# Kernel tuning notes

Measured on AMD Instinct MI355X. Metric: run time of the kernel, lower is better.

## Reference

```python
import jax, jax.numpy as jnp
import numpy as np

DIM = 1024
HEADS = 16
HEAD_DIM = DIM // HEADS
B, S = 4, 2048


def setup_inputs() -> dict:
    key = jax.random.key(0)
    ks = jax.random.split(key, 10)
    std = 1.0 / np.sqrt(DIM)
    def lin(k):
        kw, kb = jax.random.split(k)
        W = jax.random.uniform(kw, (DIM, DIM), jnp.float32, -std, std)
        b = jax.random.uniform(kb, (DIM,), jnp.float32, -std, std)
        return W, b
    Wq, bq = lin(ks[0])
    Wk, bk = lin(ks[1])
    Wv, bv = lin(ks[2])
    Wo, bo = lin(ks[3])
    q = jax.random.normal(ks[4], (B, S, DIM), jnp.float32)
    mask = jnp.ones((B, S), dtype=bool)
    return {"q": q, "mask": mask, "Wq": Wq, "bq": bq, "Wk": Wk, "bk": bk,
            "Wv": Wv, "bv": bv, "Wo": Wo, "bo": bo}


def reference(q, mask, Wq, bq, Wk, bk, Wv, bv, Wo, bo):
    # self-attention: k = v = q
    Bsz, Sq, D = q.shape
    scale = HEAD_DIM ** -0.5
    qh = (q @ Wq.T + bq).reshape(Bsz, Sq, HEADS, HEAD_DIM)
    kh = (q @ Wk.T + bk).reshape(Bsz, Sq, HEADS, HEAD_DIM)
    vh = (q @ Wv.T + bv).reshape(Bsz, Sq, HEADS, HEAD_DIM)
    # scores: [B, H, Sq, Sk]
    scores = jnp.einsum('bqhd,bkhd->bhqk', qh, kh) * scale
    neg_inf = jnp.finfo(scores.dtype).min
    # padding mask (batch, seq) -> broadcast over heads and query dim
    scores = jnp.where(mask[:, None, None, :], scores, neg_inf)
    # causal mask
    causal = jnp.triu(jnp.ones((Sq, Sq), dtype=bool), k=1)
    scores = jnp.where(causal[None, None], neg_inf, scores)
    attn = jax.nn.softmax(scores, axis=-1)
    out = jnp.einsum('bhqk,bkhd->bqhd', attn, vh).reshape(Bsz, Sq, D)
    return out @ Wo.T + bo
```

## Files before the change

kernel.cpp:

```cpp
#include <hip/hip_runtime.h>
#include <stdint.h>

#define DIM   1024
#define HEADS 16
#define HD    64
#define BATCH 4
#define SEQ   2048
#define MTOT  (BATCH*SEQ)

typedef __attribute__((ext_vector_type(8))) short bf16x8;
typedef __attribute__((ext_vector_type(4))) float f32x4;

__device__ __forceinline__ unsigned short f2bf(float x) {
    unsigned int u = __float_as_uint(x);
    unsigned int r = (u + 0x7fffu + ((u >> 16) & 1u)) >> 16;
    return (unsigned short)r;
}

__device__ __forceinline__ unsigned int pkbf(float lo, float hi) {
    return __builtin_amdgcn_perm(__float_as_uint(hi) + 0x8000u,
                                 __float_as_uint(lo) + 0x8000u, 0x07060302u);
}
__device__ __forceinline__ unsigned int pktr(float lo, float hi) {
    return __builtin_amdgcn_perm(__float_as_uint(hi),
                                 __float_as_uint(lo), 0x07060302u);
}

__device__ __forceinline__ void gload_lds16(const void* g, void* l) {
    typedef __attribute__((address_space(1))) const unsigned int gbl_uint;
    typedef __attribute__((address_space(3))) unsigned int lds_uint;
    __builtin_amdgcn_global_load_lds(
        reinterpret_cast<gbl_uint*>(reinterpret_cast<uintptr_t>(g)),
        reinterpret_cast<lds_uint*>((unsigned int)reinterpret_cast<uintptr_t>(l)),
        16, 0, 0);
}

__global__ __launch_bounds__(256)
void cast_all(const float* __restrict__ q,
              const float* __restrict__ w0, const float* __restrict__ w1,
              const float* __restrict__ w2, const float* __restrict__ w3,
              unsigned short* __restrict__ qb, unsigned short* __restrict__ wb)
{
    size_t e = ((size_t)blockIdx.x * 256 + threadIdx.x) * 4;
    const float* src; unsigned short* dst; size_t off;
    if (e < (size_t)MTOT * DIM) { src = q; dst = qb; off = e; }
    else {
        size_t we = e - (size_t)MTOT * DIM;
        int wi = (int)(we >> 20);
        off = we & 1048575u;
        src = wi == 0 ? w0 : wi == 1 ? w1 : wi == 2 ? w2 : w3;
        dst = wb + (size_t)wi * 1048576;
    }
    float4 v = *(const float4*)(src + off);
    uint2 r; r.x = pkbf(v.x, v.y); r.y = pkbf(v.z, v.w);
    *(uint2*)(dst + off) = r;
}

#define READ_A(D, MH) { \
    _Pragma("unroll") for (int i2 = 0; i2 < 4; ++i2) { \
        const unsigned short* p_ = L + (D) * 32768 + aoff + (MH) * 4096 + i2 * 1024; \
        af[i2][0] = *(const bf16x8*)(p_ + e0 * 8); \
        af[i2][1] = *(const bf16x8*)(p_ + e1 * 8); } }

#define READ_B(D, NH) { \
    _Pragma("unroll") for (int j2 = 0; j2 < 2; ++j2) { \
        const unsigned short* p_ = L + (D) * 32768 + boff + (NH) * 2048 + j2 * 1024; \
        bfr[NH][j2][0] = *(const bf16x8*)(p_ + e0 * 8); \
        bfr[NH][j2][1] = *(const bf16x8*)(p_ + e1 * 8); } }

#define MFMA_Q(MH, NH) { \
    _Pragma("unroll") for (int i2 = 0; i2 < 4; ++i2) \
    _Pragma("unroll") for (int j2 = 0; j2 < 2; ++j2) { \
        acc[(MH)*4+i2][(NH)*2+j2] = __builtin_amdgcn_mfma_f32_16x16x32_bf16( \
            af[i2][0], bfr[NH][j2][0], acc[(MH)*4+i2][(NH)*2+j2], 0, 0, 0); \
        acc[(MH)*4+i2][(NH)*2+j2] = __builtin_amdgcn_mfma_f32_16x16x32_bf16( \
            af[i2][1], bfr[NH][j2][1], acc[(MH)*4+i2][(NH)*2+j2], 0, 0, 0); } }

#define STAGE_A(D, H, TT) { \
    const unsigned short* sp_ = Ag + (size_t)(H) * 131072 + (TT) * 64; \
    unsigned short* lp_ = L + (D) * 32768 + (H) * 8192 + w * 1024; \
    gload_lds16(sp_, lp_); \
    gload_lds16(sp_ + 8192, lp_ + 512); }

#define STAGE_B(D, H, TT) { \
    const unsigned short* sp_ = Bg + (size_t)(H) * 131072 + (TT) * 64; \
    unsigned short* lp_ = L + (D) * 32768 + 16384 + (H) * 8192 + w * 1024; \
    gload_lds16(sp_, lp_); \
    gload_lds16(sp_ + 8192, lp_ + 512); }

#define VMW4 asm volatile("s_waitcnt vmcnt(4)" ::: "memory")
#define VMW0 asm volatile("s_waitcnt vmcnt(0)" ::: "memory")
#define NOSTMT ((void)0)

#define PHASE(D, MH, NH, RA, RB, STAGE_STMT, VM_STMT) { \
    if (RA) READ_A(D, MH); \
    if (RB) READ_B(D, NH); \
    STAGE_STMT; \
    __builtin_amdgcn_sched_barrier(0); \
    __builtin_amdgcn_s_barrier(); \
    asm volatile("s_waitcnt lgkmcnt(0)" ::: "memory"); \
    __builtin_amdgcn_sched_barrier(0); \
    __builtin_amdgcn_s_setprio(1); \
    MFMA_Q(MH, NH); \
    __builtin_amdgcn_s_setprio(0); \
    VM_STMT; \
    __builtin_amdgcn_sched_barrier(0); \
    __builtin_amdgcn_s_barrier(); }

template<bool OUT_F32>
__global__ __launch_bounds__(512, 2)
void gemm256(const unsigned short* __restrict__ X,
             const unsigned short* __restrict__ W0, const float* __restrict__ b0, void* __restrict__ O0,
             const unsigned short* __restrict__ W1, const float* __restrict__ b1, void* __restrict__ O1,
             const unsigned short* __restrict__ W2, const float* __restrict__ b2, void* __restrict__ O2,
             float scale0, int vt2)
{
    const unsigned short* W; const float* bias; void* Out;
    if (blockIdx.z == 0)      { W = W0; bias = b0; Out = O0; }
    else if (blockIdx.z == 1) { W = W1; bias = b1; Out = O1; }
    else                      { W = W2; bias = b2; Out = O2; }

    extern __shared__ unsigned short L[];

    const int t    = threadIdx.x;
    const int w    = t >> 6;
    const int lane = t & 63;
    const int quad = lane >> 4;
    const int l16  = lane & 15;
    const int wm   = w >> 2;
    const int wn   = w & 3;
    const int m0   = blockIdx.y * 256;
    const int n0   = blockIdx.x * 256;

    const int grow = lane >> 3;
    const size_t gOff = (size_t)(w * 16 + grow) * 1024 + ((lane & 7) ^ grow) * 8;
    const unsigned short* Ag = X + (size_t)m0 * 1024 + gOff;
    const unsigned short* Bg = W + (size_t)n0 * 1024 + gOff;

    const int e0   = quad ^ (l16 & 7);
    const int e1   = e0 ^ 4;
    const int aoff = wm * 8192 + l16 * 64;
    const int boff = 16384 + wn * 4096 + l16 * 64;

    f32x4 acc[8][4];
    #pragma unroll
    for (int i = 0; i < 8; ++i)
        #pragma unroll
        for (int j = 0; j < 4; ++j) acc[i][j] = (f32x4){0.f,0.f,0.f,0.f};

    bf16x8 af[4][2];
    bf16x8 bfr[2][2][2];

    STAGE_A(0, 0, 0); STAGE_A(0, 1, 0);
    STAGE_B(0, 0, 0); STAGE_B(0, 1, 0);
    STAGE_B(1, 0, 1); STAGE_B(1, 1, 1);
    VMW4;
    __builtin_amdgcn_s_barrier();

    for (int it = 0; it < 7; ++it) {
        const int kv = 2 * it + 1;
        PHASE(0, 0, 0, 1, 1, STAGE_A(1, 0, kv),     NOSTMT);
        PHASE(0, 0, 1, 0, 1, STAGE_A(1, 1, kv),     NOSTMT);
        PHASE(0, 1, 1, 1, 0, STAGE_B(0, 0, kv + 1), NOSTMT);
        PHASE(0, 1, 0, 0, 0, STAGE_B(0, 1, kv + 1), VMW4);
        PHASE(1, 0, 0, 1, 1, STAGE_A(0, 0, kv + 1), NOSTMT);
        PHASE(1, 0, 1, 0, 1, STAGE_A(0, 1, kv + 1), NOSTMT);
        PHASE(1, 1, 1, 1, 0, STAGE_B(1, 0, kv + 2), NOSTMT);
        PHASE(1, 1, 0, 0, 0, STAGE_B(1, 1, kv + 2), VMW4);
    }
    PHASE(0, 0, 0, 1, 1, STAGE_A(1, 0, 15), NOSTMT);
    PHASE(0, 0, 1, 0, 1, STAGE_A(1, 1, 15), NOSTMT);
    PHASE(0, 1, 1, 1, 0, NOSTMT,            NOSTMT);
    PHASE(0, 1, 0, 0, 0, NOSTMT,            VMW0);
    PHASE(1, 0, 0, 1, 1, NOSTMT,            NOSTMT);
    PHASE(1, 0, 1, 0, 1, NOSTMT,            NOSTMT);
    PHASE(1, 1, 1, 1, 0, NOSTMT,            NOSTMT);
    PHASE(1, 1, 0, 0, 0, NOSTMT,            NOSTMT);

    const float sc = (blockIdx.z == 0) ? scale0 : 1.0f;
    const bool trans = (!OUT_F32) && vt2 && (blockIdx.z == 2);

    #pragma unroll
    for (int j = 0; j < 4; ++j) {
        const int col = n0 + wn * 64 + j * 16 + l16;
        const float bv = bias[col];
        #pragma unroll
        for (int i = 0; i < 8; ++i) {
            const int rowg = m0 + wm * 128 + i * 16 + quad * 4;
            if (trans) {
                const int bb = rowg >> 11, ss = rowg & 2047;
                const int hh = col >> 6, dd = col & 63;
                uint2 pk;
                pk.x = pkbf(acc[i][j][0] + bv, acc[i][j][1] + bv);
                pk.y = pkbf(acc[i][j][2] + bv, acc[i][j][3] + bv);
                *(uint2*)((unsigned short*)Out + ((size_t)((bb * 16 + hh) * 64 + dd)) * SEQ + ss) = pk;
            } else {
                #pragma unroll
                for (int r = 0; r < 4; ++r) {
                    float v = (acc[i][j][r] + bv) * sc;
                    if (OUT_F32)
                        ((float*)Out)[(size_t)(rowg + r) * 1024 + col] = v;
                    else
                        ((unsigned short*)Out)[(size_t)(rowg + r) * 1024 + col] = f2bf(v);
                }
            }
        }
    }
}

struct Job { int qt, kt0, kt1, slot; };
__device__ const Job g_jobs[40] = {
    {3,0,8,-1},{7,0,8,6},{7,8,16,7},{10,0,8,14},
    {11,0,8,17},{11,8,16,18},{11,16,24,19},{14,0,8,28},{14,8,16,29},
    {15,0,8,32},{15,8,16,33},{15,16,24,34},{15,24,32,35},
    {6,0,7,4},{6,7,14,5},{9,0,7,11},{9,7,14,12},{10,8,15,15},{10,15,22,16},
    {12,0,7,20},{12,7,14,21},{13,0,7,24},{13,7,14,25},{13,14,21,26},{13,21,28,27},
    {14,16,23,30},{14,23,30,31},
    {2,0,6,-1},{5,0,6,2},{5,6,12,3},{8,0,6,8},{8,6,12,9},{8,12,18,10},
    {9,14,20,13},{12,14,20,22},{12,20,26,23},
    {4,0,5,0},{4,5,10,1},{1,0,4,-1},{0,0,2,-1},
};
#define NSLOT 36

__global__ __launch_bounds__(256)
void attn_mfma(const unsigned short* __restrict__ Qh,
               const unsigned short* __restrict__ Kh,
               const unsigned short* __restrict__ Vtg,
               unsigned short* __restrict__ Oh,
               unsigned short* __restrict__ Opart,
               float* __restrict__ Ml)
{
    __shared__ unsigned short Ks[64 * 72];
    __shared__ unsigned short Vs[64 * 72];
    __shared__ unsigned short Ps[128 * 72];

    const int t    = threadIdx.x;
    const int w    = t >> 6;
    const int lane = t & 63;
    const int quad = lane >> 4;
    const int l16  = lane & 15;

    const Job job = g_jobs[blockIdx.y];
    const int qt  = job.qt;
    const int bh  = blockIdx.x;
    const int b   = bh >> 4;
    const int h   = bh & 15;
    const int q0  = qt * 128;
    const size_t base  = (size_t)b * SEQ * DIM + (size_t)h * HD;
    const size_t vbase = (size_t)bh * HD * SEQ;

    bf16x8 onesf;
    #pragma unroll
    for (int e = 0; e < 8; ++e) onesf[e] = (short)0x3f80;

    bf16x8 qf[2][2];
    #pragma unroll
    for (int st = 0; st < 2; ++st) {
        const unsigned short* qp = Qh + base + (size_t)(q0 + (w * 2 + st) * 16 + l16) * DIM;
        qf[st][0] = *(const bf16x8*)(qp + quad * 8);
        qf[st][1] = *(const bf16x8*)(qp + 32 + quad * 8);
    }

    f32x4 oacc[2][4];
    f32x4 lacc[2];
    #pragma unroll
    for (int st = 0; st < 2; ++st) {
        lacc[st] = (f32x4){0.f,0.f,0.f,0.f};
        #pragma unroll
        for (int dj = 0; dj < 4; ++dj) oacc[st][dj] = (f32x4){0.f,0.f,0.f,0.f};
    }

    const int lrow = t >> 2;
    const int lcol = (t & 3) * 16;
    const unsigned short* kg = Kh + base + (size_t)lrow * DIM + lcol;
    const unsigned short* vg = Vtg + vbase + (size_t)lrow * SEQ + lcol;
    unsigned short* ksw = &Ks[lrow * 72 + lcol];
    unsigned short* vsw = &Vs[lrow * 72 + lcol];

    bf16x8 krg0, krg1, vrg0, vrg1;
    {
        const int k0p = job.kt0 * 64;
        krg0 = *(const bf16x8*)(kg + (size_t)k0p * DIM);
        krg1 = *(const bf16x8*)(kg + (size_t)k0p * DIM + 8);
        vrg0 = *(const bf16x8*)(vg + k0p);
        vrg1 = *(const bf16x8*)(vg + k0p + 8);
    }

    for (int kt = job.kt0; kt < job.kt1; ++kt) {
        const int k0 = kt * 64;
        __syncthreads();
        *(bf16x8*)ksw       = krg0;
        *(bf16x8*)(ksw + 8) = krg1;
        *(bf16x8*)vsw       = vrg0;
        *(bf16x8*)(vsw + 8) = vrg1;
        if (kt + 1 < job.kt1) {
            const int kn = k0 + 64;
            krg0 = *(const bf16x8*)(kg + (size_t)kn * DIM);
            krg1 = *(const bf16x8*)(kg + (size_t)kn * DIM + 8);
            vrg0 = *(const bf16x8*)(vg + kn);
            vrg1 = *(const bf16x8*)(vg + kn + 8);
        }
        __syncthreads();

        if (k0 > q0 + w * 32 + 31) continue;

        f32x4 scr[2][4];
        #pragma unroll
        for (int j = 0; j < 4; ++j) {
            bf16x8 kf0 = *(const bf16x8*)&Ks[(j * 16 + l16) * 72 + quad * 8];
            bf16x8 kf1 = *(const bf16x8*)&Ks[(j * 16 + l16) * 72 + 32 + quad * 8];
            #pragma unroll
            for (int st = 0; st < 2; ++st) {
                f32x4 acc0 = __builtin_amdgcn_mfma_f32_16x16x32_bf16(kf0, qf[st][0], (f32x4){0.f,0.f,0.f,0.f}, 0, 0, 0);
                scr[st][j] = __builtin_amdgcn_mfma_f32_16x16x32_bf16(kf1, qf[st][1], acc0, 0, 0, 0);
            }
        }

        #pragma unroll
        for (int st = 0; st < 2; ++st) {
            const int qs = (w * 2 + st) * 16;
            if (k0 + 63 > q0 + qs) {
                const int koff = k0 - q0 - qs + quad * 4;
                #pragma unroll
                for (int j = 0; j < 4; ++j)
                    #pragma unroll
                    for (int r = 0; r < 4; ++r)
                        if (j * 16 + koff + r > l16) scr[st][j][r] = -1e30f;
            }
            const int prow = (qs + l16) * 72;
            #pragma unroll
            for (int j = 0; j < 4; ++j) {
                float p0 = __builtin_amdgcn_exp2f(scr[st][j][0]);
                float p1 = __builtin_amdgcn_exp2f(scr[st][j][1]);
                float p2 = __builtin_amdgcn_exp2f(scr[st][j][2]);
                float p3 = __builtin_amdgcn_exp2f(scr[st][j][3]);
                uint2 pk; pk.x = pktr(p0, p1); pk.y = pktr(p2, p3);
                *(uint2*)&Ps[prow + j * 16 + quad * 4] = pk;
            }
        }

        bf16x8 pf[2][2];
        #pragma unroll
        for (int st = 0; st < 2; ++st) {
            const int prow = ((w * 2 + st) * 16 + l16) * 72;
            pf[st][0] = *(const bf16x8*)&Ps[prow + quad * 8];
            pf[st][1] = *(const bf16x8*)&Ps[prow + 32 + quad * 8];
        }
        #pragma unroll
        for (int dj = 0; dj < 4; ++dj) {
            bf16x8 vf0 = *(const bf16x8*)&Vs[(dj * 16 + l16) * 72 + quad * 8];
            bf16x8 vf1 = *(const bf16x8*)&Vs[(dj * 16 + l16) * 72 + 32 + quad * 8];
            #pragma unroll
            for (int st = 0; st < 2; ++st) {
                oacc[st][dj] = __builtin_amdgcn_mfma_f32_16x16x32_bf16(vf0, pf[st][0], oacc[st][dj], 0, 0, 0);
                oacc[st][dj] = __builtin_amdgcn_mfma_f32_16x16x32_bf16(vf1, pf[st][1], oacc[st][dj], 0, 0, 0);
            }
        }
        #pragma unroll
        for (int st = 0; st < 2; ++st) {
            lacc[st] = __builtin_amdgcn_mfma_f32_16x16x32_bf16(onesf, pf[st][0], lacc[st], 0, 0, 0);
            lacc[st] = __builtin_amdgcn_mfma_f32_16x16x32_bf16(onesf, pf[st][1], lacc[st], 0, 0, 0);
        }
    }

    if (job.slot < 0) {
        #pragma unroll
        for (int st = 0; st < 2; ++st) {
            const float inv = __builtin_amdgcn_rcpf(lacc[st][0]);
            const size_t orow = base + (size_t)(q0 + (w * 2 + st) * 16 + l16) * DIM;
            #pragma unroll
            for (int dj = 0; dj < 4; ++dj) {
                uint2 pk;
                pk.x = pkbf(oacc[st][dj][0] * inv, oacc[st][dj][1] * inv);
                pk.y = pkbf(oacc[st][dj][2] * inv, oacc[st][dj][3] * inv);
                *(uint2*)&Oh[orow + dj * 16 + quad * 4] = pk;
            }
        }
    } else {
        const size_t sb = ((size_t)bh * NSLOT + job.slot) * 128;
        #pragma unroll
        for (int st = 0; st < 2; ++st) {
            const int rl = (w * 2 + st) * 16 + l16;
            unsigned short* op = Opart + (sb + rl) * 64;
            #pragma unroll
            for (int dj = 0; dj < 4; ++dj) {
                uint2 pk;
                pk.x = pkbf(oacc[st][dj][0], oacc[st][dj][1]);
                pk.y = pkbf(oacc[st][dj][2], oacc[st][dj][3]);
                *(uint2*)(op + dj * 16 + quad * 4) = pk;
            }
            if (quad == 0) Ml[sb + rl] = lacc[st][0];
        }
    }
}

__device__ const int c_slotBase[12] = {0,2,4,6,8,11,14,17,20,24,28,32};
__device__ const int c_nparts[12]  = {2,2,2,2,3,3,3,3,4,4,4,4};

__global__ __launch_bounds__(256)
void attn_combine(const unsigned short* __restrict__ Opart, const float* __restrict__ Ml,
                  unsigned short* __restrict__ Oh)
{
    const int idx = blockIdx.x * 256 + threadIdx.x;
    const int d4  = idx & 15;
    const int r   = (idx >> 4) & 127;
    const int rest = idx >> 11;
    const int qti = rest % 12;
    const int bh  = rest / 12;
    const int np  = c_nparts[qti];
    const size_t sb = (size_t)bh * NSLOT + c_slotBase[qti];

    float o0 = 0.f, o1 = 0.f, o2 = 0.f, o3 = 0.f, l = 0.f;
    for (int p = 0; p < np; ++p) {
        const size_t rb = (sb + p) * 128 + r;
        uint2 pk = *(const uint2*)(Opart + rb * 64 + d4 * 4);
        o0 += __uint_as_float(pk.x << 16);
        o1 += __uint_as_float(pk.x & 0xffff0000u);
        o2 += __uint_as_float(pk.y << 16);
        o3 += __uint_as_float(pk.y & 0xffff0000u);
        l  += Ml[rb];
    }
    const float inv = __builtin_amdgcn_rcpf(l);
    const int b = bh >> 4, h = bh & 15;
    const int qq = (qti + 4) * 128 + r;
    uint2 outp;
    outp.x = pkbf(o0 * inv, o1 * inv);
    outp.y = pkbf(o2 * inv, o3 * inv);
    *(uint2*)&Oh[(size_t)b * SEQ * DIM + (size_t)qq * DIM + h * 64 + d4 * 4] = outp;
}

extern "C" void kernel_launch(void* const* d_in, const int* in_sizes, int n_in,
                              void* d_out, int out_size, void* d_ws, size_t ws_size,
                              hipStream_t stream)
{
    const float* q  = (const float*)d_in[0];
    const float* Wq = (const float*)d_in[2];
    const float* bq = (const float*)d_in[3];
    const float* Wk = (const float*)d_in[4];
    const float* bk = (const float*)d_in[5];
    const float* Wv = (const float*)d_in[6];
    const float* bv = (const float*)d_in[7];
    const float* Wo = (const float*)d_in[8];
    const float* bo = (const float*)d_in[9];

    unsigned short* qb  = (unsigned short*)d_ws;
    unsigned short* Wqb = qb  + (size_t)MTOT * DIM;
    unsigned short* Wkb = Wqb + (size_t)DIM * DIM;
    unsigned short* Wvb = Wkb + (size_t)DIM * DIM;
    unsigned short* Wob = Wvb + (size_t)DIM * DIM;
    unsigned short* qh  = Wob + (size_t)DIM * DIM;
    unsigned short* kh  = qh  + (size_t)MTOT * DIM;
    unsigned short* vt  = kh  + (size_t)MTOT * DIM;
    unsigned short* ao  = vt  + (size_t)MTOT * DIM;
    unsigned short* Opart = ao + (size_t)MTOT * DIM;
    float* Ml = (float*)qb;

    static bool s_attr_done = false;
    if (!s_attr_done) {
        hipFuncSetAttribute(reinterpret_cast<const void*>(&gemm256<false>),
                            hipFuncAttributeMaxDynamicSharedMemorySize, 131072);
        hipFuncSetAttribute(reinterpret_cast<const void*>(&gemm256<true>),
                            hipFuncAttributeMaxDynamicSharedMemorySize, 131072);
        s_attr_done = true;
    }

    dim3 blk(256);

    hipLaunchKernelGGL(cast_all, dim3((MTOT * DIM + 4 * DIM * DIM) / 1024), blk, 0, stream,
                       q, Wq, Wk, Wv, Wo, qb, Wqb);

    dim3 g1(DIM / 256, MTOT / 256, 3);
    hipLaunchKernelGGL((gemm256<false>), g1, dim3(512), 131072, stream,
                       qb, Wqb, bq, (void*)qh, Wkb, bk, (void*)kh, Wvb, bv, (void*)vt,
                       0.125f * 1.44269504089f, 1);

    dim3 g2(BATCH * HEADS, 40);
    hipLaunchKernelGGL(attn_mfma, g2, blk, 0, stream, qh, kh, vt, ao, Opart, Ml);

    hipLaunchKernelGGL(attn_combine, dim3((64 * 12 * 128 * 16) / 256), blk, 0, stream,
                       Opart, Ml, ao);

    dim3 g3(DIM / 256, MTOT / 256, 1);
    hipLaunchKernelGGL((gemm256<true>), g3, dim3(512), 131072, stream,
                       ao, Wob, bo, d_out, Wob, bo, d_out, Wob, bo, d_out,
                       1.0f, 0);
}
```

Before: 276.0 us.

## Split-K output projection, reorder GEMM prefetch schedule, raise attention MFMA priority

```diff
diff --git a/kernel.cpp b/kernel.cpp
--- a/kernel.cpp
+++ b/kernel.cpp
@@ -88,7 +88,7 @@
     gload_lds16(sp_, lp_); \
     gload_lds16(sp_ + 8192, lp_ + 512); }
 
-#define VMW4 asm volatile("s_waitcnt vmcnt(4)" ::: "memory")
+#define VMW6 asm volatile("s_waitcnt vmcnt(6)" ::: "memory")
 #define VMW0 asm volatile("s_waitcnt vmcnt(0)" ::: "memory")
 #define NOSTMT ((void)0)
 
@@ -107,18 +107,19 @@
     __builtin_amdgcn_sched_barrier(0); \
     __builtin_amdgcn_s_barrier(); }
 
-template<bool OUT_F32>
+template<int MODE, int NT>
 __global__ __launch_bounds__(512, 2)
 void gemm256(const unsigned short* __restrict__ X,
              const unsigned short* __restrict__ W0, const float* __restrict__ b0, void* __restrict__ O0,
              const unsigned short* __restrict__ W1, const float* __restrict__ b1, void* __restrict__ O1,
              const unsigned short* __restrict__ W2, const float* __restrict__ b2, void* __restrict__ O2,
-             float scale0, int vt2)
+             float scale0, int vt2, int kofs)
 {
     const unsigned short* W; const float* bias; void* Out;
     if (blockIdx.z == 0)      { W = W0; bias = b0; Out = O0; }
     else if (blockIdx.z == 1) { W = W1; bias = b1; Out = O1; }
     else                      { W = W2; bias = b2; Out = O2; }
+    const int zoff = (MODE == 1) ? (int)blockIdx.z * kofs : 0;
 
     extern __shared__ unsigned short L[];
 
@@ -134,8 +135,8 @@
 
     const int grow = lane >> 3;
     const size_t gOff = (size_t)(w * 16 + grow) * 1024 + ((lane & 7) ^ grow) * 8;
-    const unsigned short* Ag = X + (size_t)m0 * 1024 + gOff;
-    const unsigned short* Bg = W + (size_t)n0 * 1024 + gOff;
+    const unsigned short* Ag = X + (size_t)m0 * 1024 + zoff + gOff;
+    const unsigned short* Bg = W + (size_t)n0 * 1024 + zoff + gOff;
 
     const int e0   = quad ^ (l16 & 7);
     const int e1   = e0 ^ 4;
@@ -154,36 +155,38 @@
     STAGE_A(0, 0, 0); STAGE_A(0, 1, 0);
     STAGE_B(0, 0, 0); STAGE_B(0, 1, 0);
     STAGE_B(1, 0, 1); STAGE_B(1, 1, 1);
-    VMW4;
+    STAGE_A(1, 0, 1);
+    VMW6;
     __builtin_amdgcn_s_barrier();
 
-    for (int it = 0; it < 7; ++it) {
+    for (int it = 0; it < NT / 2 - 1; ++it) {
         const int kv = 2 * it + 1;
-        PHASE(0, 0, 0, 1, 1, STAGE_A(1, 0, kv),     NOSTMT);
-        PHASE(0, 0, 1, 0, 1, STAGE_A(1, 1, kv),     NOSTMT);
-        PHASE(0, 1, 1, 1, 0, STAGE_B(0, 0, kv + 1), NOSTMT);
-        PHASE(0, 1, 0, 0, 0, STAGE_B(0, 1, kv + 1), VMW4);
-        PHASE(1, 0, 0, 1, 1, STAGE_A(0, 0, kv + 1), NOSTMT);
-        PHASE(1, 0, 1, 0, 1, STAGE_A(0, 1, kv + 1), NOSTMT);
-        PHASE(1, 1, 1, 1, 0, STAGE_B(1, 0, kv + 2), NOSTMT);
-        PHASE(1, 1, 0, 0, 0, STAGE_B(1, 1, kv + 2), VMW4);
-    }
-    PHASE(0, 0, 0, 1, 1, STAGE_A(1, 0, 15), NOSTMT);
-    PHASE(0, 0, 1, 0, 1, STAGE_A(1, 1, 15), NOSTMT);
-    PHASE(0, 1, 1, 1, 0, NOSTMT,            NOSTMT);
-    PHASE(0, 1, 0, 0, 0, NOSTMT,            VMW0);
-    PHASE(1, 0, 0, 1, 1, NOSTMT,            NOSTMT);
-    PHASE(1, 0, 1, 0, 1, NOSTMT,            NOSTMT);
-    PHASE(1, 1, 1, 1, 0, NOSTMT,            NOSTMT);
-    PHASE(1, 1, 0, 0, 0, NOSTMT,            NOSTMT);
+        PHASE(0, 0, 0, 1, 1, STAGE_A(1, 1, kv),     NOSTMT);
+        PHASE(0, 0, 1, 0, 1, STAGE_B(0, 0, kv + 1), NOSTMT);
+        PHASE(0, 1, 1, 1, 0, STAGE_B(0, 1, kv + 1), NOSTMT);
+        PHASE(0, 1, 0, 0, 0, STAGE_A(0, 0, kv + 1), VMW6);
+        PHASE(1, 0, 0, 1, 1, STAGE_A(0, 1, kv + 1), NOSTMT);
+        PHASE(1, 0, 1, 0, 1, NOSTMT,                NOSTMT);
+        PHASE(1, 1, 1, 1, 0,
+              { STAGE_B(1, 0, kv + 2); STAGE_B(1, 1, kv + 2); }, NOSTMT);
+        PHASE(1, 1, 0, 0, 0, STAGE_A(1, 0, kv + 2), VMW6);
+    }
+    PHASE(0, 0, 0, 1, 1, STAGE_A(1, 1, NT - 1), NOSTMT);
+    PHASE(0, 0, 1, 0, 1, NOSTMT,                NOSTMT);
+    PHASE(0, 1, 1, 1, 0, NOSTMT,                NOSTMT);
+    PHASE(0, 1, 0, 0, 0, NOSTMT,                VMW0);
+    PHASE(1, 0, 0, 1, 1, NOSTMT,                NOSTMT);
+    PHASE(1, 0, 1, 0, 1, NOSTMT,                NOSTMT);
+    PHASE(1, 1, 1, 1, 0, NOSTMT,                NOSTMT);
+    PHASE(1, 1, 0, 0, 0, NOSTMT,                NOSTMT);
 
     const float sc = (blockIdx.z == 0) ? scale0 : 1.0f;
-    const bool trans = (!OUT_F32) && vt2 && (blockIdx.z == 2);
+    const bool trans = (MODE == 0) && vt2 && (blockIdx.z == 2);
 
     #pragma unroll
     for (int j = 0; j < 4; ++j) {
         const int col = n0 + wn * 64 + j * 16 + l16;
-        const float bv = bias[col];
+        const float bv = (MODE == 0) ? bias[col] : 0.f;
         #pragma unroll
         for (int i = 0; i < 8; ++i) {
             const int rowg = m0 + wm * 128 + i * 16 + quad * 4;
@@ -194,18 +197,32 @@
                 pk.x = pkbf(acc[i][j][0] + bv, acc[i][j][1] + bv);
                 pk.y = pkbf(acc[i][j][2] + bv, acc[i][j][3] + bv);
                 *(uint2*)((unsigned short*)Out + ((size_t)((bb * 16 + hh) * 64 + dd)) * SEQ + ss) = pk;
+            } else if (MODE == 1) {
+                #pragma unroll
+                for (int r = 0; r < 4; ++r)
+                    ((float*)Out)[(size_t)(rowg + r) * 1024 + col] = acc[i][j][r];
             } else {
                 #pragma unroll
                 for (int r = 0; r < 4; ++r) {
                     float v = (acc[i][j][r] + bv) * sc;
-                    if (OUT_F32)
-                        ((float*)Out)[(size_t)(rowg + r) * 1024 + col] = v;
-                    else
-                        ((unsigned short*)Out)[(size_t)(rowg + r) * 1024 + col] = f2bf(v);
+                    ((unsigned short*)Out)[(size_t)(rowg + r) * 1024 + col] = f2bf(v);
                 }
             }
         }
     }
+}
+
+__global__ __launch_bounds__(256)
+void oproj_combine(const float* __restrict__ P0, const float* __restrict__ P1,
+                   const float* __restrict__ bo, float* __restrict__ out)
+{
+    size_t i = ((size_t)blockIdx.x * 256 + threadIdx.x) * 4;
+    float4 a = *(const float4*)(P0 + i);
+    float4 b = *(const float4*)(P1 + i);
+    float4 c = *(const float4*)(bo + (i & 1023));
+    float4 r; r.x = a.x + b.x + c.x; r.y = a.y + b.y + c.y;
+    r.z = a.z + b.z + c.z; r.w = a.w + b.w + c.w;
+    *(float4*)(out + i) = r;
 }
 
 struct Job { int qt, kt0, kt1, slot; };
@@ -304,6 +321,8 @@
 
         if (k0 > q0 + w * 32 + 31) continue;
 
+        __builtin_amdgcn_s_setprio(1);
+
         f32x4 scr[2][4];
         #pragma unroll
         for (int j = 0; j < 4; ++j) {
@@ -361,6 +380,8 @@
             lacc[st] = __builtin_amdgcn_mfma_f32_16x16x32_bf16(onesf, pf[st][0], lacc[st], 0, 0, 0);
             lacc[st] = __builtin_amdgcn_mfma_f32_16x16x32_bf16(onesf, pf[st][1], lacc[st], 0, 0, 0);
         }
+
+        __builtin_amdgcn_s_setprio(0);
     }
 
     if (job.slot < 0) {
@@ -454,12 +475,14 @@
     unsigned short* ao  = vt  + (size_t)MTOT * DIM;
     unsigned short* Opart = ao + (size_t)MTOT * DIM;
     float* Ml = (float*)qb;
+    float* P0 = (float*)kh;
+    float* P1 = (float*)Opart;
 
     static bool s_attr_done = false;
     if (!s_attr_done) {
-        hipFuncSetAttribute(reinterpret_cast<const void*>(&gemm256<false>),
+        hipFuncSetAttribute(reinterpret_cast<const void*>(&gemm256<0,16>),
                             hipFuncAttributeMaxDynamicSharedMemorySize, 131072);
-        hipFuncSetAttribute(reinterpret_cast<const void*>(&gemm256<true>),
+        hipFuncSetAttribute(reinterpret_cast<const void*>(&gemm256<1,8>),
                             hipFuncAttributeMaxDynamicSharedMemorySize, 131072);
         s_attr_done = true;
     }
@@ -470,9 +493,9 @@
                        q, Wq, Wk, Wv, Wo, qb, Wqb);
 
     dim3 g1(DIM / 256, MTOT / 256, 3);
-    hipLaunchKernelGGL((gemm256<false>), g1, dim3(512), 131072, stream,
+    hipLaunchKernelGGL((gemm256<0,16>), g1, dim3(512), 131072, stream,
                        qb, Wqb, bq, (void*)qh, Wkb, bk, (void*)kh, Wvb, bv, (void*)vt,
-                       0.125f * 1.44269504089f, 1);
+                       0.125f * 1.44269504089f, 1, 0);
 
     dim3 g2(BATCH * HEADS, 40);
     hipLaunchKernelGGL(attn_mfma, g2, blk, 0, stream, qh, kh, vt, ao, Opart, Ml);
@@ -480,8 +503,11 @@
     hipLaunchKernelGGL(attn_combine, dim3((64 * 12 * 128 * 16) / 256), blk, 0, stream,
                        Opart, Ml, ao);
 
-    dim3 g3(DIM / 256, MTOT / 256, 1);
-    hipLaunchKernelGGL((gemm256<true>), g3, dim3(512), 131072, stream,
-                       ao, Wob, bo, d_out, Wob, bo, d_out, Wob, bo, d_out,
-                       1.0f, 0);
-}
+    dim3 g3(DIM / 256, MTOT / 256, 2);
+    hipLaunchKernelGGL((gemm256<1,8>), g3, dim3(512), 131072, stream,
+                       ao, Wob, nullptr, (void*)P0, Wob, nullptr, (void*)P1,
+                       Wob, nullptr, nullptr, 1.0f, 0, 512);
+
+    hipLaunchKernelGGL(oproj_combine, dim3((MTOT * DIM) / 1024), blk, 0, stream,
+                       P0, P1, bo, (float*)d_out);
+}
```

After: 293.0 us. +6.2%, slower.
